# Kernel optimization log

Measured on AMD Instinct MI355X. Metric: run time of the kernel, lower is better.

## Reference

```python
import jax, jax.numpy as jnp
import numpy as np

B, S, T = 32, 128, 64
H = 512
VS = VT = 32000


def _lstm_cell(x, h, c, W, U, b):
    # Keras LSTM gate order: i, f, g(cell), o
    z = x @ W + h @ U + b
    i, f, g, o = jnp.split(z, 4, axis=-1)
    c = jax.nn.sigmoid(f) * c + jax.nn.sigmoid(i) * jnp.tanh(g)
    h = jax.nn.sigmoid(o) * jnp.tanh(c)
    return h, c


def _lstm_scan(xs, h0, c0, W, U, b):
    # xs: [S, B, D]
    def step(carry, x):
        h, c = _lstm_cell(x, carry[0], carry[1], W, U, b)
        return (h, c), h
    (hT, cT), hs = jax.lax.scan(step, (h0, c0), xs)
    return hs, hT, cT


def setup_inputs() -> dict:
    key = jax.random.key(0)
    ks = jax.random.split(key, 16)
    def n(k, shape, s=0.02):
        return (jax.random.normal(k, shape, jnp.float32) * s).astype(jnp.float32)
    return {
        "src": jax.random.randint(ks[0], (B, S), 0, VS, jnp.int32),
        "trg": jax.random.randint(ks[1], (B, T), 0, VT, jnp.int32),
        "E_src": n(ks[2], (VS, H)),
        "E_trg": n(ks[3], (VT, H)),
        "Wf": n(ks[4], (H, 4 * H)), "Uf": n(ks[5], (H, 4 * H)), "bf": jnp.zeros((4 * H,), jnp.float32),
        "Wb": n(ks[6], (H, 4 * H)), "Ub": n(ks[7], (H, 4 * H)), "bb": jnp.zeros((4 * H,), jnp.float32),
        "Wd": n(ks[8], (H, 4 * H)), "Ud": n(ks[9], (H, 4 * H)), "bd": jnp.zeros((4 * H,), jnp.float32),
        "fcW": n(ks[10], (2 * H, H)), "fcb": jnp.zeros((H,), jnp.float32),
        "clsW": n(ks[11], (2 * H, VT)), "clsb": jnp.zeros((VT,), jnp.float32),
    }


def reference(src, trg, E_src, E_trg, Wf, Uf, bf, Wb, Ub, bb, Wd, Ud, bd, fcW, fcb, clsW, clsb):
    Bn = src.shape[0]
    Hn = E_src.shape[1]
    # --- Encoder: bidirectional LSTM ---
    xs = E_src[src].transpose(1, 0, 2)          # [S, B, H]
    z0 = jnp.zeros((Bn, Hn), xs.dtype)
    hs_f, hf, cf = _lstm_scan(xs, z0, z0, Wf, Uf, bf)
    hs_b, hb, cb = _lstm_scan(xs[::-1], z0, z0, Wb, Ub, bb)
    src_hidden = jnp.concatenate([hs_f, hs_b[::-1]], axis=-1).transpose(1, 0, 2)  # [B, S, 2H]
    # --- shared fc projections (same Dense, 2H -> H) ---
    src_h = src_hidden @ fcW + fcb                                   # [B, S, H]
    prev_h = jnp.concatenate([hf, hb], axis=-1) @ fcW + fcb          # [B, H]
    prev_c = jnp.concatenate([cf, cb], axis=-1) @ fcW + fcb          # [B, H]
    neg = jnp.where(src == 0, jnp.float32(-1e9), jnp.float32(0.0))   # [B, S]
    # --- Decoder (teacher forcing): per-step LSTM cell + dot-product attention ---
    ys = E_trg[trg[:, :-1]].transpose(1, 0, 2)  # [T-1, B, H]

    def step(carry, x):
        h, c = _lstm_cell(x, carry[0], carry[1], Wd, Ud, bd)
        score = jnp.einsum('bh,bsh->bs', h, src_h) + neg
        attn = jax.nn.softmax(score, axis=-1)
        ws = jnp.einsum('bs,bsh->bh', attn, src_h)
        return (h, c), jnp.concatenate([ws, h], axis=-1)  # dec_state [B, 2H]

    _, dec = jax.lax.scan(step, (prev_h, prev_c), ys)     # [T-1, B, 2H]
    logits = dec.transpose(1, 0, 2) @ clsW + clsb          # [B, T-1, VT]
    return logits
```

## Files before the change

### kernel.cpp

```cpp
#include <hip/hip_runtime.h>
#include <hip/hip_bf16.h>
#include <stdint.h>
#include <string.h>

constexpr int cB = 32, cS = 128, cT = 64, cH = 512, cH4 = 2048, cVT = 32000, cTM1 = 63;

typedef __attribute__((ext_vector_type(8))) __bf16 bf16x8;
typedef __attribute__((ext_vector_type(4))) float f32x4;

__device__ __forceinline__ float sigm(float x) { return 1.0f / (1.0f + expf(-x)); }

__device__ __forceinline__ bf16x8 sc_load16(const __hip_bfloat16* p) {
  bf16x8 r;
  asm volatile("global_load_dwordx4 %0, %1, off sc0 sc1"
               : "=&v"(r) : "v"(p) : "memory");
  return r;
}
__device__ __forceinline__ void sc_store4(__hip_bfloat16* p, unsigned v) {
  asm volatile("global_store_dword %0, %1, off sc0 sc1"
               :: "v"(p), "v"(v) : "memory");
}
__device__ __forceinline__ void pl_store4(__hip_bfloat16* p, unsigned v) {
  asm volatile("global_store_dword %0, %1, off"
               :: "v"(p), "v"(v) : "memory");
}

__device__ __forceinline__ void gridbar_nw(unsigned* ctr, unsigned* flag,
                                           unsigned nblk, unsigned gen) {
  __builtin_amdgcn_sched_barrier(0);
  __builtin_amdgcn_s_barrier();
  if (threadIdx.x == 0) {
    unsigned old = __hip_atomic_fetch_add(ctr, 1u, __ATOMIC_RELAXED,
                                          __HIP_MEMORY_SCOPE_AGENT);
    if (old == gen * nblk - 1u) {
      __hip_atomic_store(flag, gen, __ATOMIC_RELAXED, __HIP_MEMORY_SCOPE_AGENT);
    } else {
      while (__hip_atomic_load(flag, __ATOMIC_RELAXED, __HIP_MEMORY_SCOPE_AGENT) < gen)
        __builtin_amdgcn_s_sleep(1);
    }
  }
  __builtin_amdgcn_s_barrier();
  __builtin_amdgcn_sched_barrier(0);
}

__global__ __launch_bounds__(64) void k_init_bars(unsigned* p) {
  if (threadIdx.x < 16) p[threadIdx.x] = 0u;
}

__global__ __launch_bounds__(128) void k_embed_src(const int* __restrict__ src,
                                                   const float* __restrict__ E,
                                                   __hip_bfloat16* __restrict__ xs_bf,
                                                   float* __restrict__ neg) {
  int sb = blockIdx.x;
  int s = sb >> 5, b = sb & 31;
  int tok = src[b * cS + s];
  float4 e = ((const float4*)(E + (size_t)tok * cH))[threadIdx.x];
  __hip_bfloat16* drow = xs_bf + (size_t)sb * cH + threadIdx.x * 4;
  drow[0] = __float2bfloat16(e.x); drow[1] = __float2bfloat16(e.y);
  drow[2] = __float2bfloat16(e.z); drow[3] = __float2bfloat16(e.w);
  if (threadIdx.x == 0) neg[b * cS + s] = (tok == 0) ? -1e9f : 0.0f;
}

__global__ __launch_bounds__(128) void k_embed_trg(const int* __restrict__ trg,
                                                   const float* __restrict__ E,
                                                   __hip_bfloat16* __restrict__ ys_bf) {
  int tb = blockIdx.x;
  int t = tb >> 5, b = tb & 31;
  int tok = trg[b * cT + t];
  float4 e = ((const float4*)(E + (size_t)tok * cH))[threadIdx.x];
  __hip_bfloat16* drow = ys_bf + (size_t)tb * cH + threadIdx.x * 4;
  drow[0] = __float2bfloat16(e.x); drow[1] = __float2bfloat16(e.y);
  drow[2] = __float2bfloat16(e.z); drow[3] = __float2bfloat16(e.w);
}

__device__ __forceinline__ void f2bT_tile(const float* __restrict__ src,
                                          __hip_bfloat16* __restrict__ dst,
                                          int K, int N, int gi, int bx, int by,
                                          float (*t)[33]) {
  int nt = bx * 32, kt = by * 32;
  int c = threadIdx.x & 31, r0 = threadIdx.x >> 5;
#pragma unroll
  for (int i = 0; i < 4; ++i) {
    int r = r0 + i * 8;
    t[r][c] = src[(size_t)(kt + r) * N + nt + c];
  }
  __syncthreads();
#pragma unroll
  for (int i = 0; i < 4; ++i) {
    int row = nt + r0 + i * 8;
    int pr = gi ? (((row & 511) << 2) | (row >> 9)) : row;
    dst[(size_t)pr * K + kt + c] = __float2bfloat16(t[c][r0 + i * 8]);
  }
  __syncthreads();
}

__global__ __launch_bounds__(256) void k_prep(
    const float* __restrict__ Wf, const float* __restrict__ Wb, const float* __restrict__ Wd,
    const float* __restrict__ Uf, const float* __restrict__ Ub, const float* __restrict__ Ud,
    const float* __restrict__ fcW,
    const float* __restrict__ bf, const float* __restrict__ bb, const float* __restrict__ bd,
    __hip_bfloat16* __restrict__ Wtfx, __hip_bfloat16* __restrict__ Wtbx,
    __hip_bfloat16* __restrict__ Wtdx,
    __hip_bfloat16* __restrict__ Utf, __hip_bfloat16* __restrict__ Utb,
    __hip_bfloat16* __restrict__ Utd,
    __hip_bfloat16* __restrict__ fcWt,
    float* __restrict__ bfx, float* __restrict__ bbx, float* __restrict__ bdx,
    __hip_bfloat16* __restrict__ ys_pad) {
  __shared__ float t[32][33];
  int id = blockIdx.x;
  if (id < 6144) {
    int grp = id >> 10, r = id & 1023;
    const float* s; __hip_bfloat16* d;
    switch (grp) {
      case 0: s = Wf; d = Wtfx; break;
      case 1: s = Wb; d = Wtbx; break;
      case 2: s = Wd; d = Wtdx; break;
      case 3: s = Uf; d = Utf; break;
      case 4: s = Ub; d = Utb; break;
      default: s = Ud; d = Utd; break;
    }
    f2bT_tile(s, d, 512, 2048, 1, r & 63, r >> 6, t);
  } else if (id < 6656) {
    int r = id - 6144;
    f2bT_tile(fcW, fcWt, 1024, 512, 0, r & 15, r >> 4, t);
  } else if (id < 6680) {
    int r = id - 6656;
    const float* s = (r < 8) ? bf : ((r < 16) ? bb : bd);
    float* d = (r < 8) ? bfx : ((r < 16) ? bbx : bdx);
    int i = (r & 7) * 256 + threadIdx.x;
    d[i] = s[(i & 3) * 512 + (i >> 2)];
  } else {
    int r = id - 6680;
    ys_pad[r * 256 + threadIdx.x] = __float2bfloat16(0.0f);
  }
}

__global__ __launch_bounds__(256) void k_bgemm(const __hip_bfloat16* __restrict__ A,
                                               const __hip_bfloat16* __restrict__ Bt,
                                               const float* __restrict__ bias,
                                               float* __restrict__ C,
                                               int M, int K, int N) {
  __shared__ __hip_bfloat16 As[128 * 64];
  __shared__ __hip_bfloat16 Bs[128 * 64];
  const int tid = threadIdx.x;
  const int lane = tid & 63;
  const int wave = tid >> 6;
  const int wr = wave >> 1, wc = wave & 1;
  const int bm = blockIdx.x * 128, bn = blockIdx.y * 128;

  f32x4 acc[4][4] = {};

  const int srow = lane >> 3;
  const int scol = (lane & 7) * 8;

  for (int kt = 0; kt < K; kt += 64) {
#pragma unroll
    for (int i = 0; i < 4; ++i) {
      int c = wave * 4 + i;
      const __hip_bfloat16* ga = A + (size_t)(bm + c * 8 + srow) * K + kt + scol;
      __builtin_amdgcn_global_load_lds(
          (const __attribute__((address_space(1))) uint32_t*)ga,
          (__attribute__((address_space(3))) uint32_t*)(As + c * 512), 16, 0, 0);
      const __hip_bfloat16* gb = Bt + (size_t)(bn + c * 8 + srow) * K + kt + scol;
      __builtin_amdgcn_global_load_lds(
          (const __attribute__((address_space(1))) uint32_t*)gb,
          (__attribute__((address_space(3))) uint32_t*)(Bs + c * 512), 16, 0, 0);
    }
    __syncthreads();

#pragma unroll
    for (int kk = 0; kk < 64; kk += 32) {
      const int ko = kk + (lane >> 4) * 8;
      bf16x8 a[4], b[4];
      const int ar = wr * 64 + (lane & 15);
#pragma unroll
      for (int m = 0; m < 4; ++m)
        a[m] = *(const bf16x8*)(As + (size_t)(ar + m * 16) * 64 + ko);
      const int br = wc * 64 + (lane & 15);
#pragma unroll
      for (int n = 0; n < 4; ++n)
        b[n] = *(const bf16x8*)(Bs + (size_t)(br + n * 16) * 64 + ko);
#pragma unroll
      for (int m = 0; m < 4; ++m)
#pragma unroll
        for (int n = 0; n < 4; ++n)
          acc[m][n] = __builtin_amdgcn_mfma_f32_16x16x32_bf16(a[m], b[n], acc[m][n], 0, 0, 0);
    }
    __syncthreads();
  }

#pragma unroll
  for (int m = 0; m < 4; ++m) {
    const int row0 = bm + wr * 64 + m * 16 + (lane >> 4) * 4;
#pragma unroll
    for (int n = 0; n < 4; ++n) {
      const int col = bn + wc * 64 + n * 16 + (lane & 15);
      const float bv = bias[col];
#pragma unroll
      for (int r = 0; r < 4; ++r) {
        const int row = row0 + r;
        if (row < M) C[(size_t)row * N + col] = acc[m][n][r] + bv;
      }
    }
  }
}

#define ENC_STEP(T, ZI0, ZI1, ZO0, ZO1)                                          \
  {                                                                              \
    const int t = (T);                                                           \
    const int trow = dir ? (127 - t) : t;                                        \
    if (t > 0) {                                                                 \
      const __hip_bfloat16* hsrc = hcur + (size_t)((t + 1) & 1) * 16384;         \
      bf16x8 hr[8];                                                              \
      _Pragma("unroll")                                                          \
      for (int i = 0; i < 8; ++i) {                                              \
        int c = tid + i * 256;                                                   \
        hr[i] = sc_load16(hsrc + (size_t)c * 8);                                 \
      }                                                                          \
      asm volatile("s_waitcnt vmcnt(0)" ::: "memory");                           \
      __builtin_amdgcn_sched_barrier(0);                                         \
      _Pragma("unroll")                                                          \
      for (int i = 0; i < 8; ++i) {                                              \
        int c = tid + i * 256;                                                   \
        int r = c >> 6, cc = (c & 63) * 8;                                       \
        *(bf16x8*)&Hs[r][cc] = hr[i];                                            \
      }                                                                          \
      asm volatile("s_waitcnt lgkmcnt(0)" ::: "memory");                         \
      __builtin_amdgcn_s_barrier();                                              \
      __builtin_amdgcn_sched_barrier(0);                                         \
    }                                                                            \
    f32x4 acc0 = {}, acc1 = {};                                                  \
    if (t > 0) {                                                                 \
      _Pragma("unroll")                                                          \
      for (int kk = 0; kk < 16; ++kk) {                                          \
        bf16x8 h0v = *(const bf16x8*)&Hs[b0][kk * 32 + fq * 8];                  \
        bf16x8 h1v = *(const bf16x8*)&Hs[b1][kk * 32 + fq * 8];                  \
        acc0 = __builtin_amdgcn_mfma_f32_16x16x32_bf16(afrag[kk], h0v, acc0, 0, 0, 0); \
        acc1 = __builtin_amdgcn_mfma_f32_16x16x32_bf16(afrag[kk], h1v, acc1, 0, 0, 0); \
      }                                                                          \
    }                                                                            \
    {                                                                            \
      float zi = ZI0[0] + acc0[0], zf = ZI0[1] + acc0[1],                        \
            zg = ZI0[2] + acc0[2], zo = ZI0[3] + acc0[3];                        \
      cs0 = sigm(zf) * cs0 + sigm(zi) * tanhf(zg);                               \
      Ho[b0][jloc] = __float2bfloat16(sigm(zo) * tanhf(cs0));                    \
    }                                                                            \
    {                                                                            \
      float zi = ZI1[0] + acc1[0], zf = ZI1[1] + acc1[1],                        \
            zg = ZI1[2] + acc1[2], zo = ZI1[3] + acc1[3];                        \
      cs1 = sigm(zf) * cs1 + sigm(zi) * tanhf(zg);                               \
      Ho[b1][jloc] = __float2bfloat16(sigm(zo) * tanhf(cs1));                    \
    }                                                                            \
    asm volatile("s_waitcnt lgkmcnt(0)" ::: "memory");                           \
    __builtin_amdgcn_s_barrier();                                                \
    __builtin_amdgcn_sched_barrier(0);                                           \
    {                                                                            \
      unsigned v = *(const unsigned*)&Ho[bb][jp];                                \
      sc_store4(hcur + (size_t)(t & 1) * 16384 + (size_t)bb * 512 + nb * 16 + jp, v); \
      pl_store4(hs + ((size_t)trow * 32 + bb) * 512 + nb * 16 + jp, v);          \
    }                                                                            \
    __builtin_amdgcn_sched_barrier(0);                                           \
    const int tn = (t < 127) ? t + 1 : 127;                                      \
    const int ntrow = dir ? (127 - tn) : tn;                                     \
    ZO0 = *(const f32x4*)(xW + ((size_t)(ntrow * 32 + b0)) * 2048 + zc);         \
    ZO1 = *(const f32x4*)(xW + ((size_t)(ntrow * 32 + b1)) * 2048 + zc);         \
    if (t < 127) {                                                               \
      asm volatile("s_waitcnt vmcnt(2)" ::: "memory");                           \
      gridbar_nw(ctr, flag, 32u, (unsigned)(t + 1));                             \
    }                                                                            \
  }

__global__ __launch_bounds__(256, 1) void k_enc_mfma(
    const float* __restrict__ xWf, const float* __restrict__ xWb,
    const __hip_bfloat16* __restrict__ Utf, const __hip_bfloat16* __restrict__ Utb,
    __hip_bfloat16* __restrict__ hs_f, __hip_bfloat16* __restrict__ hs_b,
    __hip_bfloat16* __restrict__ henc,
    float* __restrict__ cf, float* __restrict__ cb,
    unsigned* bars) {
  const int bid = blockIdx.x;
  const int dir = bid >> 5, nb = bid & 31;
  const int c0 = nb * 64;
  const float* xW = dir ? xWb : xWf;
  const __hip_bfloat16* Ut = dir ? Utb : Utf;
  __hip_bfloat16* hs = dir ? hs_b : hs_f;
  __hip_bfloat16* hcur = henc + (size_t)dir * 32768;
  float* cOut = dir ? cb : cf;
  unsigned* ctr = bars + dir * 2;
  unsigned* flag = bars + dir * 2 + 1;

  __shared__ __hip_bfloat16 Hs[32][520];
  __shared__ __hip_bfloat16 Ho[32][20];

  const int tid = threadIdx.x;
  const int lane = tid & 63;
  const int wv = tid >> 6;
  const int fr = lane & 15;
  const int fq = lane >> 4;

  bf16x8 afrag[16];
#pragma unroll
  for (int kk = 0; kk < 16; ++kk)
    afrag[kk] = *(const bf16x8*)(Ut + (size_t)(c0 + wv * 16 + fr) * 512 + kk * 32 + fq * 8);

  const int jglob = nb * 16 + wv * 4 + fq;
  const int jloc = wv * 4 + fq;
  const int b0 = fr, b1 = fr + 16;
  const int zc = c0 + wv * 16 + fq * 4;
  const int bb = tid >> 3, jp = (tid & 7) * 2;
  float cs0 = 0.f, cs1 = 0.f;

  const int trow0 = dir ? 127 : 0;
  f32x4 zA0 = *(const f32x4*)(xW + ((size_t)(trow0 * 32 + b0)) * 2048 + zc);
  f32x4 zA1 = *(const f32x4*)(xW + ((size_t)(trow0 * 32 + b1)) * 2048 + zc);
  f32x4 zB0, zB1;

  for (int it = 0; it < 64; ++it) {
    ENC_STEP(2 * it, zA0, zA1, zB0, zB1);
    ENC_STEP(2 * it + 1, zB0, zB1, zA0, zA1);
  }
  cOut[(size_t)b0 * 512 + jglob] = cs0;
  cOut[(size_t)b1 * 512 + jglob] = cs1;
}

#define DEC_STEP(T, ZI0, ZI1, ZO0, ZO1)                                          \
  {                                                                              \
    const int t = (T);                                                           \
    if (t == 0) {                                                                \
      const float4* ph4 = (const float4*)prev_h;                                 \
      _Pragma("unroll")                                                          \
      for (int i = 0; i < 16; ++i) {                                             \
        int c = tid + i * 256;                                                   \
        float4 v = ph4[c];                                                       \
        int r = c >> 7, c4 = (c & 127) * 4;                                      \
        Hs[r][c4 + 0] = __float2bfloat16(v.x);                                   \
        Hs[r][c4 + 1] = __float2bfloat16(v.y);                                   \
        Hs[r][c4 + 2] = __float2bfloat16(v.z);                                   \
        Hs[r][c4 + 3] = __float2bfloat16(v.w);                                   \
      }                                                                          \
    } else {                                                                     \
      const __hip_bfloat16* hsrc = hdec + (size_t)((t + 1) & 1) * 16384;         \
      bf16x8 hr[8];                                                              \
      _Pragma("unroll")                                                          \
      for (int i = 0; i < 8; ++i) {                                              \
        int c = tid + i * 256;                                                   \
        hr[i] = sc_load16(hsrc + (size_t)c * 8);                                 \
      }                                                                          \
      asm volatile("s_waitcnt vmcnt(0)" ::: "memory");                           \
      __builtin_amdgcn_sched_barrier(0);                                         \
      _Pragma("unroll")                                                          \
      for (int i = 0; i < 8; ++i) {                                              \
        int c = tid + i * 256;                                                   \
        int r = c >> 6, cc = (c & 63) * 8;                                       \
        *(bf16x8*)&Hs[r][cc] = hr[i];                                            \
      }                                                                          \
    }                                                                            \
    asm volatile("s_waitcnt lgkmcnt(0)" ::: "memory");                           \
    __builtin_amdgcn_s_barrier();                                                \
    __builtin_amdgcn_sched_barrier(0);                                           \
    f32x4 acc0 = {}, acc1 = {};                                                  \
    _Pragma("unroll")                                                            \
    for (int kk = 0; kk < 16; ++kk) {                                            \
      bf16x8 h0v = *(const bf16x8*)&Hs[b0][kk * 32 + fq * 8];                    \
      bf16x8 h1v = *(const bf16x8*)&Hs[b1][kk * 32 + fq * 8];                    \
      acc0 = __builtin_amdgcn_mfma_f32_16x16x32_bf16(afrag[kk], h0v, acc0, 0, 0, 0); \
      acc1 = __builtin_amdgcn_mfma_f32_16x16x32_bf16(afrag[kk], h1v, acc1, 0, 0, 0); \
    }                                                                            \
    {                                                                            \
      float zi = ZI0[0] + acc0[0], zf = ZI0[1] + acc0[1],                        \
            zg = ZI0[2] + acc0[2], zo = ZI0[3] + acc0[3];                        \
      cs0 = sigm(zf) * cs0 + sigm(zi) * tanhf(zg);                               \
      Ho[b0][jloc] = __float2bfloat16(sigm(zo) * tanhf(cs0));                    \
    }                                                                            \
    {                                                                            \
      float zi = ZI1[0] + acc1[0], zf = ZI1[1] + acc1[1],                        \
            zg = ZI1[2] + acc1[2], zo = ZI1[3] + acc1[3];                        \
      cs1 = sigm(zf) * cs1 + sigm(zi) * tanhf(zg);                               \
      Ho[b1][jloc] = __float2bfloat16(sigm(zo) * tanhf(cs1));                    \
    }                                                                            \
    asm volatile("s_waitcnt lgkmcnt(0)" ::: "memory");                           \
    __builtin_amdgcn_s_barrier();                                                \
    __builtin_amdgcn_sched_barrier(0);                                           \
    {                                                                            \
      unsigned v = *(const unsigned*)&Ho[bb][jp];                                \
      sc_store4(hdec + (size_t)(t & 1) * 16384 + (size_t)bb * 512 + nb * 16 + jp, v); \
      pl_store4(decb + ((size_t)bb * cTM1 + t) * 1024 + 512 + nb * 16 + jp, v);  \
    }                                                                            \
    __builtin_amdgcn_sched_barrier(0);                                           \
    const int tn = (t < cTM1 - 1) ? t + 1 : cTM1 - 1;                            \
    ZO0 = *(const f32x4*)(yW + ((size_t)(tn * 32 + b0)) * 2048 + zc);            \
    ZO1 = *(const f32x4*)(yW + ((size_t)(tn * 32 + b1)) * 2048 + zc);            \
    if (t < cTM1 - 1) {                                                          \
      asm volatile("s_waitcnt vmcnt(2)" ::: "memory");                           \
      gridbar_nw(ctr, flag, 32u, (unsigned)(t + 1));                             \
    }                                                                            \
  }

__global__ __launch_bounds__(256, 1) void k_dec_mfma(
    const float* __restrict__ yW, const __hip_bfloat16* __restrict__ Utd,
    const float* __restrict__ prev_h, const float* __restrict__ prev_c,
    __hip_bfloat16* __restrict__ hdec, __hip_bfloat16* __restrict__ decb,
    const float* __restrict__ clsW, __hip_bfloat16* __restrict__ clsWt,
    unsigned* ctr, unsigned* flag) {
  __shared__ __hip_bfloat16 Hs[32][520];
  __shared__ __hip_bfloat16 Ho[32][20];
  __shared__ float tcv[32][33];

  if (blockIdx.x >= 32) {
    for (int tile = blockIdx.x - 32; tile < 32000; tile += (int)gridDim.x - 32) {
      int bx = tile % 1000, by = tile / 1000;
      f2bT_tile(clsW, clsWt, 1024, 32000, 0, bx, by, tcv);
    }
    return;
  }

  const int nb = blockIdx.x;
  const int c0 = nb * 64;
  const int tid = threadIdx.x;
  const int lane = tid & 63;
  const int wv = tid >> 6;
  const int fr = lane & 15;
  const int fq = lane >> 4;

  bf16x8 afrag[16];
#pragma unroll
  for (int kk = 0; kk < 16; ++kk)
    afrag[kk] = *(const bf16x8*)(Utd + (size_t)(c0 + wv * 16 + fr) * 512 + kk * 32 + fq * 8);

  const int jglob = nb * 16 + wv * 4 + fq;
  const int jloc = wv * 4 + fq;
  const int b0 = fr, b1 = fr + 16;
  const int zc = c0 + wv * 16 + fq * 4;
  const int bb = tid >> 3, jp = (tid & 7) * 2;
  float cs0 = prev_c[(size_t)b0 * 512 + jglob];
  float cs1 = prev_c[(size_t)b1 * 512 + jglob];

  f32x4 zA0 = *(const f32x4*)(yW + ((size_t)b0) * 2048 + zc);
  f32x4 zA1 = *(const f32x4*)(yW + ((size_t)b1) * 2048 + zc);
  f32x4 zB0, zB1;

  for (int it = 0; it < 31; ++it) {
    DEC_STEP(2 * it, zA0, zA1, zB0, zB1);
    DEC_STEP(2 * it + 1, zB0, zB1, zA0, zA1);
  }
  DEC_STEP(62, zA0, zA1, zB0, zB1);
}

__global__ __launch_bounds__(128) void k_cat_bf(const __hip_bfloat16* __restrict__ hs_f,
                                                const __hip_bfloat16* __restrict__ hs_b,
                                                const float* __restrict__ cf,
                                                const float* __restrict__ cb,
                                                __hip_bfloat16* __restrict__ cat) {
  int r = blockIdx.x;
  int tid = threadIdx.x;
  __hip_bfloat16* drow = cat + (size_t)r * 1024 + tid * 8;
  if (r >= 4160) {
    bf16x8 zv = {};
    *(bf16x8*)drow = zv;
    return;
  }
  if (r < 4128) {
    const __hip_bfloat16 *pf, *pb;
    if (r < 4096) {
      int b = r >> 7, s = r & 127;
      pf = hs_f + ((size_t)s * 32 + b) * 512;
      pb = hs_b + ((size_t)s * 32 + b) * 512;
    } else {
      int b = r - 4096;
      pf = hs_f + ((size_t)127 * 32 + b) * 512;
      pb = hs_b + ((size_t)b) * 512;
    }
    const __hip_bfloat16* s8 = (tid < 64) ? (pf + tid * 8) : (pb + (tid - 64) * 8);
    *(bf16x8*)drow = *(const bf16x8*)s8;
  } else {
    int b = r - 4128;
    const float* s8 = (tid < 64) ? (cf + (size_t)b * 512 + tid * 8)
                                 : (cb + (size_t)b * 512 + (tid - 64) * 8);
    bf16x8 v;
#pragma unroll
    for (int i = 0; i < 8; ++i) v[i] = (__bf16)s8[i];
    *(bf16x8*)drow = v;
  }
}

__global__ __launch_bounds__(256) void k_attn_all(const float* __restrict__ src_h,
                                                  const float* __restrict__ neg,
                                                  __hip_bfloat16* __restrict__ decb) {
  int bid = blockIdx.x;
  int xcd = bid & 7, idx = bid >> 3;
  int b = xcd + 8 * (idx / 63);
  int t = idx % 63;
  int tx = threadIdx.x;
  __shared__ float hv[cH];
  __shared__ float part[256];
  __shared__ float sc[cS];
  __shared__ float red[cS];
  __hip_bfloat16* drow = decb + ((size_t)b * cTM1 + t) * (2 * cH);
  hv[tx] = __bfloat162float(drow[cH + tx]);
  hv[tx + 256] = __bfloat162float(drow[cH + tx + 256]);
  __syncthreads();
  {
    int s = tx >> 1, half = tx & 1;
    const float4* sr = (const float4*)(src_h + ((size_t)b * cS + s) * cH + half * 256);
    const float4* hh = (const float4*)(hv + half * 256);
    float acc = 0.f;
#pragma unroll 8
    for (int k = 0; k < 64; ++k) {
      float4 v = sr[k], h4 = hh[k];
      acc += v.x * h4.x + v.y * h4.y + v.z * h4.z + v.w * h4.w;
    }
    part[tx] = acc;
  }
  __syncthreads();
  if (tx < cS) {
    float s0 = part[2 * tx] + part[2 * tx + 1] + neg[b * cS + tx];
    sc[tx] = s0;
    red[tx] = s0;
  }
  __syncthreads();
  for (int off = 64; off >= 1; off >>= 1) {
    if (tx < off) red[tx] = fmaxf(red[tx], red[tx + off]);
    __syncthreads();
  }
  float mx = red[0];
  __syncthreads();
  float e = 0.f;
  if (tx < cS) { e = expf(sc[tx] - mx); red[tx] = e; }
  __syncthreads();
  for (int off = 64; off >= 1; off >>= 1) {
    if (tx < off) red[tx] += red[tx + off];
    __syncthreads();
  }
  float inv = 1.0f / red[0];
  __syncthreads();
  if (tx < cS) sc[tx] = e * inv;
  __syncthreads();
  float a0 = 0.f, a1 = 0.f;
  for (int s = 0; s < cS; ++s) {
    float w = sc[s];
    const float* sr = src_h + ((size_t)b * cS + s) * cH;
    a0 += w * sr[tx];
    a1 += w * sr[tx + 256];
  }
  drow[tx] = __float2bfloat16(a0);
  drow[tx + 256] = __float2bfloat16(a1);
}

extern "C" void kernel_launch(void* const* d_in, const int* in_sizes, int n_in,
                              void* d_out, int out_size, void* d_ws, size_t ws_size,
                              hipStream_t stream) {
  const int* src = (const int*)d_in[0];
  const int* trg = (const int*)d_in[1];
  const float* E_src = (const float*)d_in[2];
  const float* E_trg = (const float*)d_in[3];
  const float* Wf = (const float*)d_in[4];
  const float* Uf = (const float*)d_in[5];
  const float* bf = (const float*)d_in[6];
  const float* Wb = (const float*)d_in[7];
  const float* Ub = (const float*)d_in[8];
  const float* bb = (const float*)d_in[9];
  const float* Wd = (const float*)d_in[10];
  const float* Ud = (const float*)d_in[11];
  const float* bd = (const float*)d_in[12];
  const float* fcW = (const float*)d_in[13];
  const float* fcb = (const float*)d_in[14];
  const float* clsW = (const float*)d_in[15];
  const float* clsb = (const float*)d_in[16];
  float* out = (float*)d_out;
  float* ws = (float*)d_ws;

  float* xWf = ws;
  float* xWb = ws + 8388608;
  float* yW = ws + 16777216;
  __hip_bfloat16* hs_f = (__hip_bfloat16*)(ws + 20905984);
  __hip_bfloat16* hs_b = (__hip_bfloat16*)(ws + 21954560);
  float* cf = ws + 23003136;
  float* cb = ws + 23019520;
  float* neg = ws + 23035904;
  float* fco = ws + 23040000;
  __hip_bfloat16* decb = (__hip_bfloat16*)(ws + 25169920);
  __hip_bfloat16* Utd = (__hip_bfloat16*)(ws + 26218496);
  __hip_bfloat16* henc = (__hip_bfloat16*)(ws + 26742784);
  __hip_bfloat16* hdec = (__hip_bfloat16*)(ws + 26808320);
  unsigned* bars = (unsigned*)(ws + 26841088);
  float* pool = ws + 26841152;

  __hip_bfloat16* xs_bf = (__hip_bfloat16*)pool;
  __hip_bfloat16* ys_bf = (__hip_bfloat16*)(pool + 1048576);
  __hip_bfloat16* Utf = (__hip_bfloat16*)(pool + 1572864);
  __hip_bfloat16* Utb = (__hip_bfloat16*)(pool + 2097152);
  __hip_bfloat16* Wtfx = (__hip_bfloat16*)(pool + 2621440);
  __hip_bfloat16* Wtbx = (__hip_bfloat16*)(pool + 3145728);
  __hip_bfloat16* Wtdx = (__hip_bfloat16*)(pool + 3670016);
  float* bfx = pool + 4194304;
  float* bbx = pool + 4196352;
  float* bdx = pool + 4198400;
  __hip_bfloat16* fcWt = (__hip_bfloat16*)(pool + 4200448);
  __hip_bfloat16* cat_bf = (__hip_bfloat16*)pool;
  __hip_bfloat16* clsWt = (__hip_bfloat16*)xWf;

  k_embed_src<<<4096, 128, 0, stream>>>(src, E_src, xs_bf, neg);
  k_embed_trg<<<2016, 128, 0, stream>>>(trg, E_trg, ys_bf);
  k_prep<<<6744, 256, 0, stream>>>(Wf, Wb, Wd, Uf, Ub, Ud, fcW, bf, bb, bd,
                                   Wtfx, Wtbx, Wtdx, Utf, Utb, Utd, fcWt,
                                   bfx, bbx, bdx, ys_bf + (size_t)2016 * 512);

  k_bgemm<<<dim3(32, 16), 256, 0, stream>>>(xs_bf, Wtfx, bfx, xWf, 4096, 512, 2048);
  k_bgemm<<<dim3(32, 16), 256, 0, stream>>>(xs_bf, Wtbx, bbx, xWb, 4096, 512, 2048);
  k_bgemm<<<dim3(16, 16), 256, 0, stream>>>(ys_bf, Wtdx, bdx, yW, 2016, 512, 2048);

  k_init_bars<<<1, 64, 0, stream>>>(bars);
  k_enc_mfma<<<64, 256, 0, stream>>>(xWf, xWb, Utf, Utb, hs_f, hs_b, henc, cf, cb, bars);

  k_cat_bf<<<4224, 128, 0, stream>>>(hs_f, hs_b, cf, cb, cat_bf);
  k_bgemm<<<dim3(33, 4), 256, 0, stream>>>(cat_bf, fcWt, fcb, fco, 4160, 1024, 512);

  const float* prev_h = fco + (size_t)4096 * 512;
  const float* prev_c = fco + (size_t)4128 * 512;
  k_dec_mfma<<<256, 256, 0, stream>>>(yW, Utd, prev_h, prev_c, hdec, decb,
                                      clsW, clsWt, bars + 4, bars + 5);
  k_attn_all<<<2016, 256, 0, stream>>>(fco, neg, decb);

  k_bgemm<<<dim3(16, 250), 256, 0, stream>>>(decb, clsWt, clsb, out, 2016, 1024, 32000);
}
```

Baseline: 1.243 ms.

## Halve recurrent LSTM blocks to 512 threads and use per-block slot barriers

The encoder and decoder recurrent kernels now run 16 blocks per direction with 512 threads each instead of 32 blocks with 256 threads, so each block owns 32 hidden units. The shared atomic-counter grid barrier is replaced by a slot barrier: each block writes its generation to its own slot, and one wave polls all 16 slots with coherent loads. Fewer participants and no atomic contention are meant to cut the per-timestep synchronisation latency on the serial recurrence, at the cost of more work per block on the critical path. The clsW transpose helper is also adapted to 512-thread blocks.

```diff
diff --git a/kernel.cpp b/kernel.cpp
--- a/kernel.cpp
+++ b/kernel.cpp
@@ -24,27 +24,20 @@
   asm volatile("global_store_dword %0, %1, off"
                :: "v"(p), "v"(v) : "memory");
 }
-
-__device__ __forceinline__ void gridbar_nw(unsigned* ctr, unsigned* flag,
-                                           unsigned nblk, unsigned gen) {
-  __builtin_amdgcn_sched_barrier(0);
-  __builtin_amdgcn_s_barrier();
-  if (threadIdx.x == 0) {
-    unsigned old = __hip_atomic_fetch_add(ctr, 1u, __ATOMIC_RELAXED,
-                                          __HIP_MEMORY_SCOPE_AGENT);
-    if (old == gen * nblk - 1u) {
-      __hip_atomic_store(flag, gen, __ATOMIC_RELAXED, __HIP_MEMORY_SCOPE_AGENT);
-    } else {
-      while (__hip_atomic_load(flag, __ATOMIC_RELAXED, __HIP_MEMORY_SCOPE_AGENT) < gen)
-        __builtin_amdgcn_s_sleep(1);
-    }
-  }
-  __builtin_amdgcn_s_barrier();
-  __builtin_amdgcn_sched_barrier(0);
+__device__ __forceinline__ unsigned sc_loadu(const unsigned* p) {
+  unsigned r;
+  asm volatile("global_load_dword %0, %1, off sc0 sc1"
+               : "=&v"(r) : "v"(p) : "memory");
+  asm volatile("s_waitcnt vmcnt(0)" ::: "memory");
+  return r;
+}
+__device__ __forceinline__ void sc_storeu(unsigned* p, unsigned v) {
+  asm volatile("global_store_dword %0, %1, off sc0 sc1"
+               :: "v"(p), "v"(v) : "memory");
 }
 
 __global__ __launch_bounds__(64) void k_init_bars(unsigned* p) {
-  if (threadIdx.x < 16) p[threadIdx.x] = 0u;
+  p[threadIdx.x] = 0u;
 }
 
 __global__ __launch_bounds__(128) void k_embed_src(const int* __restrict__ src,
@@ -90,6 +83,26 @@
     int row = nt + r0 + i * 8;
     int pr = gi ? (((row & 511) << 2) | (row >> 9)) : row;
     dst[(size_t)pr * K + kt + c] = __float2bfloat16(t[c][r0 + i * 8]);
+  }
+  __syncthreads();
+}
+
+__device__ __forceinline__ void f2bT_tile512(const float* __restrict__ src,
+                                             __hip_bfloat16* __restrict__ dst,
+                                             int K, int N, int bx, int by,
+                                             float (*t)[33]) {
+  int nt = bx * 32, kt = by * 32;
+  int c = threadIdx.x & 31, r0 = (threadIdx.x >> 5) & 15;
+#pragma unroll
+  for (int i = 0; i < 2; ++i) {
+    int r = r0 + i * 16;
+    t[r][c] = src[(size_t)(kt + r) * N + nt + c];
+  }
+  __syncthreads();
+#pragma unroll
+  for (int i = 0; i < 2; ++i) {
+    int row = nt + r0 + i * 16;
+    dst[(size_t)row * K + kt + c] = __float2bfloat16(t[c][r0 + i * 16]);
   }
   __syncthreads();
 }
@@ -205,23 +218,40 @@
   }
 }
 
+#define SLOT_BARRIER(SLOTS, NB, GEN)                                             \
+  {                                                                              \
+    asm volatile("s_waitcnt vmcnt(2)" ::: "memory");                             \
+    __builtin_amdgcn_sched_barrier(0);                                           \
+    __builtin_amdgcn_s_barrier();                                                \
+    if (tid == 0) sc_storeu((SLOTS) + (NB), (unsigned)(GEN));                    \
+    if (wv == 0) {                                                               \
+      for (;;) {                                                                 \
+        unsigned v = sc_loadu((SLOTS) + (lane & 15));                            \
+        if (__all((lane >= 16) | (v >= (unsigned)(GEN)))) break;                 \
+        __builtin_amdgcn_s_sleep(1);                                             \
+      }                                                                          \
+    }                                                                            \
+    __builtin_amdgcn_s_barrier();                                                \
+    __builtin_amdgcn_sched_barrier(0);                                           \
+  }
+
 #define ENC_STEP(T, ZI0, ZI1, ZO0, ZO1)                                          \
   {                                                                              \
     const int t = (T);                                                           \
     const int trow = dir ? (127 - t) : t;                                        \
     if (t > 0) {                                                                 \
       const __hip_bfloat16* hsrc = hcur + (size_t)((t + 1) & 1) * 16384;         \
-      bf16x8 hr[8];                                                              \
+      bf16x8 hr[4];                                                              \
       _Pragma("unroll")                                                          \
-      for (int i = 0; i < 8; ++i) {                                              \
-        int c = tid + i * 256;                                                   \
+      for (int i = 0; i < 4; ++i) {                                              \
+        int c = tid + i * 512;                                                   \
         hr[i] = sc_load16(hsrc + (size_t)c * 8);                                 \
       }                                                                          \
       asm volatile("s_waitcnt vmcnt(0)" ::: "memory");                           \
       __builtin_amdgcn_sched_barrier(0);                                         \
       _Pragma("unroll")                                                          \
-      for (int i = 0; i < 8; ++i) {                                              \
-        int c = tid + i * 256;                                                   \
+      for (int i = 0; i < 4; ++i) {                                              \
+        int c = tid + i * 512;                                                   \
         int r = c >> 6, cc = (c & 63) * 8;                                       \
         *(bf16x8*)&Hs[r][cc] = hr[i];                                            \
       }                                                                          \
@@ -256,40 +286,36 @@
     __builtin_amdgcn_sched_barrier(0);                                           \
     {                                                                            \
       unsigned v = *(const unsigned*)&Ho[bb][jp];                                \
-      sc_store4(hcur + (size_t)(t & 1) * 16384 + (size_t)bb * 512 + nb * 16 + jp, v); \
-      pl_store4(hs + ((size_t)trow * 32 + bb) * 512 + nb * 16 + jp, v);          \
+      sc_store4(hcur + (size_t)(t & 1) * 16384 + (size_t)bb * 512 + nb * 32 + jp, v); \
+      pl_store4(hs + ((size_t)trow * 32 + bb) * 512 + nb * 32 + jp, v);          \
     }                                                                            \
     __builtin_amdgcn_sched_barrier(0);                                           \
     const int tn = (t < 127) ? t + 1 : 127;                                      \
     const int ntrow = dir ? (127 - tn) : tn;                                     \
     ZO0 = *(const f32x4*)(xW + ((size_t)(ntrow * 32 + b0)) * 2048 + zc);         \
     ZO1 = *(const f32x4*)(xW + ((size_t)(ntrow * 32 + b1)) * 2048 + zc);         \
-    if (t < 127) {                                                               \
-      asm volatile("s_waitcnt vmcnt(2)" ::: "memory");                           \
-      gridbar_nw(ctr, flag, 32u, (unsigned)(t + 1));                             \
-    }                                                                            \
-  }
-
-__global__ __launch_bounds__(256, 1) void k_enc_mfma(
+    if (t < 127) SLOT_BARRIER(slots, nb, t + 1);                                 \
+  }
+
+__global__ __launch_bounds__(512, 1) void k_enc_mfma(
     const float* __restrict__ xWf, const float* __restrict__ xWb,
     const __hip_bfloat16* __restrict__ Utf, const __hip_bfloat16* __restrict__ Utb,
     __hip_bfloat16* __restrict__ hs_f, __hip_bfloat16* __restrict__ hs_b,
     __hip_bfloat16* __restrict__ henc,
     float* __restrict__ cf, float* __restrict__ cb,
     unsigned* bars) {
+  __shared__ __hip_bfloat16 Hs[32][520];
+  __shared__ __hip_bfloat16 Ho[32][36];
+
   const int bid = blockIdx.x;
-  const int dir = bid >> 5, nb = bid & 31;
-  const int c0 = nb * 64;
+  const int dir = bid >> 4, nb = bid & 15;
+  const int c0 = nb * 128;
   const float* xW = dir ? xWb : xWf;
   const __hip_bfloat16* Ut = dir ? Utb : Utf;
   __hip_bfloat16* hs = dir ? hs_b : hs_f;
   __hip_bfloat16* hcur = henc + (size_t)dir * 32768;
   float* cOut = dir ? cb : cf;
-  unsigned* ctr = bars + dir * 2;
-  unsigned* flag = bars + dir * 2 + 1;
-
-  __shared__ __hip_bfloat16 Hs[32][520];
-  __shared__ __hip_bfloat16 Ho[32][20];
+  unsigned* slots = bars + dir * 16;
 
   const int tid = threadIdx.x;
   const int lane = tid & 63;
@@ -302,11 +328,11 @@
   for (int kk = 0; kk < 16; ++kk)
     afrag[kk] = *(const bf16x8*)(Ut + (size_t)(c0 + wv * 16 + fr) * 512 + kk * 32 + fq * 8);
 
-  const int jglob = nb * 16 + wv * 4 + fq;
+  const int jglob = nb * 32 + wv * 4 + fq;
   const int jloc = wv * 4 + fq;
   const int b0 = fr, b1 = fr + 16;
   const int zc = c0 + wv * 16 + fq * 4;
-  const int bb = tid >> 3, jp = (tid & 7) * 2;
+  const int bb = tid >> 4, jp = (tid & 15) * 2;
   float cs0 = 0.f, cs1 = 0.f;
 
   const int trow0 = dir ? 127 : 0;
@@ -328,8 +354,8 @@
     if (t == 0) {                                                                \
       const float4* ph4 = (const float4*)prev_h;                                 \
       _Pragma("unroll")                                                          \
-      for (int i = 0; i < 16; ++i) {                                             \
-        int c = tid + i * 256;                                                   \
+      for (int i = 0; i < 8; ++i) {                                              \
+        int c = tid + i * 512;                                                   \
         float4 v = ph4[c];                                                       \
         int r = c >> 7, c4 = (c & 127) * 4;                                      \
         Hs[r][c4 + 0] = __float2bfloat16(v.x);                                   \
@@ -339,17 +365,17 @@
       }                                                                          \
     } else {                                                                     \
       const __hip_bfloat16* hsrc = hdec + (size_t)((t + 1) & 1) * 16384;         \
-      bf16x8 hr[8];                                                              \
+      bf16x8 hr[4];                                                              \
       _Pragma("unroll")                                                          \
-      for (int i = 0; i < 8; ++i) {                                              \
-        int c = tid + i * 256;                                                   \
+      for (int i = 0; i < 4; ++i) {                                              \
+        int c = tid + i * 512;                                                   \
         hr[i] = sc_load16(hsrc + (size_t)c * 8);                                 \
       }                                                                          \
       asm volatile("s_waitcnt vmcnt(0)" ::: "memory");                           \
       __builtin_amdgcn_sched_barrier(0);                                         \
       _Pragma("unroll")                                                          \
-      for (int i = 0; i < 8; ++i) {                                              \
-        int c = tid + i * 256;                                                   \
+      for (int i = 0; i < 4; ++i) {                                              \
+        int c = tid + i * 512;                                                   \
         int r = c >> 6, cc = (c & 63) * 8;                                       \
         *(bf16x8*)&Hs[r][cc] = hr[i];                                            \
       }                                                                          \
@@ -382,39 +408,36 @@
     __builtin_amdgcn_sched_barrier(0);                                           \
     {                                                                            \
       unsigned v = *(const unsigned*)&Ho[bb][jp];                                \
-      sc_store4(hdec + (size_t)(t & 1) * 16384 + (size_t)bb * 512 + nb * 16 + jp, v); \
-      pl_store4(decb + ((size_t)bb * cTM1 + t) * 1024 + 512 + nb * 16 + jp, v);  \
+      sc_store4(hdec + (size_t)(t & 1) * 16384 + (size_t)bb * 512 + nb * 32 + jp, v); \
+      pl_store4(decb + ((size_t)bb * cTM1 + t) * 1024 + 512 + nb * 32 + jp, v);  \
     }                                                                            \
     __builtin_amdgcn_sched_barrier(0);                                           \
     const int tn = (t < cTM1 - 1) ? t + 1 : cTM1 - 1;                            \
     ZO0 = *(const f32x4*)(yW + ((size_t)(tn * 32 + b0)) * 2048 + zc);            \
     ZO1 = *(const f32x4*)(yW + ((size_t)(tn * 32 + b1)) * 2048 + zc);            \
-    if (t < cTM1 - 1) {                                                          \
-      asm volatile("s_waitcnt vmcnt(2)" ::: "memory");                           \
-      gridbar_nw(ctr, flag, 32u, (unsigned)(t + 1));                             \
-    }                                                                            \
-  }
-
-__global__ __launch_bounds__(256, 1) void k_dec_mfma(
+    if (t < cTM1 - 1) SLOT_BARRIER(slots, nb, t + 1);                            \
+  }
+
+__global__ __launch_bounds__(512, 1) void k_dec_mfma(
     const float* __restrict__ yW, const __hip_bfloat16* __restrict__ Utd,
     const float* __restrict__ prev_h, const float* __restrict__ prev_c,
     __hip_bfloat16* __restrict__ hdec, __hip_bfloat16* __restrict__ decb,
     const float* __restrict__ clsW, __hip_bfloat16* __restrict__ clsWt,
-    unsigned* ctr, unsigned* flag) {
+    unsigned* slots) {
   __shared__ __hip_bfloat16 Hs[32][520];
-  __shared__ __hip_bfloat16 Ho[32][20];
+  __shared__ __hip_bfloat16 Ho[32][36];
   __shared__ float tcv[32][33];
 
-  if (blockIdx.x >= 32) {
-    for (int tile = blockIdx.x - 32; tile < 32000; tile += (int)gridDim.x - 32) {
+  if (blockIdx.x >= 16) {
+    for (int tile = blockIdx.x - 16; tile < 32000; tile += (int)gridDim.x - 16) {
       int bx = tile % 1000, by = tile / 1000;
-      f2bT_tile(clsW, clsWt, 1024, 32000, 0, bx, by, tcv);
+      f2bT_tile512(clsW, clsWt, 1024, 32000, bx, by, tcv);
     }
     return;
   }
 
   const int nb = blockIdx.x;
-  const int c0 = nb * 64;
+  const int c0 = nb * 128;
   const int tid = threadIdx.x;
   const int lane = tid & 63;
   const int wv = tid >> 6;
@@ -426,11 +449,11 @@
   for (int kk = 0; kk < 16; ++kk)
     afrag[kk] = *(const bf16x8*)(Utd + (size_t)(c0 + wv * 16 + fr) * 512 + kk * 32 + fq * 8);
 
-  const int jglob = nb * 16 + wv * 4 + fq;
+  const int jglob = nb * 32 + wv * 4 + fq;
   const int jloc = wv * 4 + fq;
   const int b0 = fr, b1 = fr + 16;
   const int zc = c0 + wv * 16 + fq * 4;
-  const int bb = tid >> 3, jp = (tid & 7) * 2;
+  const int bb = tid >> 4, jp = (tid & 15) * 2;
   float cs0 = prev_c[(size_t)b0 * 512 + jglob];
   float cs1 = prev_c[(size_t)b1 * 512 + jglob];
 
@@ -609,15 +632,15 @@
   k_bgemm<<<dim3(16, 16), 256, 0, stream>>>(ys_bf, Wtdx, bdx, yW, 2016, 512, 2048);
 
   k_init_bars<<<1, 64, 0, stream>>>(bars);
-  k_enc_mfma<<<64, 256, 0, stream>>>(xWf, xWb, Utf, Utb, hs_f, hs_b, henc, cf, cb, bars);
+  k_enc_mfma<<<32, 512, 0, stream>>>(xWf, xWb, Utf, Utb, hs_f, hs_b, henc, cf, cb, bars);
 
   k_cat_bf<<<4224, 128, 0, stream>>>(hs_f, hs_b, cf, cb, cat_bf);
   k_bgemm<<<dim3(33, 4), 256, 0, stream>>>(cat_bf, fcWt, fcb, fco, 4160, 1024, 512);
 
   const float* prev_h = fco + (size_t)4096 * 512;
   const float* prev_c = fco + (size_t)4128 * 512;
-  k_dec_mfma<<<256, 256, 0, stream>>>(yW, Utd, prev_h, prev_c, hdec, decb,
-                                      clsW, clsWt, bars + 4, bars + 5);
+  k_dec_mfma<<<256, 512, 0, stream>>>(yW, Utd, prev_h, prev_c, hdec, decb,
+                                      clsW, clsWt, bars + 32);
   k_attn_all<<<2016, 256, 0, stream>>>(fco, neg, decb);
 
   k_bgemm<<<dim3(16, 250), 256, 0, stream>>>(decb, clsWt, clsb, out, 2016, 1024, 32000);
```

Measured after the change: 1.208 ms. 1.03x faster.
